# Optimization experiments

Measured on AMD Instinct MI355X. Metric: run time of the kernel, lower is better.

The kernel has to match this reference:

```python
import jax, jax.numpy as jnp
import numpy as np

# ---- dims derived from Decoder(input_size=64, hidden_size=64, output_size=64, n_units=512) ----
B, L, I = 512, 256, 64
N_UNITS, N_MOTOR = 512, 64
N_COMMAND = max(int(0.4 * (N_UNITS - N_MOTOR)), 1)   # 179 (AutoNCP rule)
N_INTER = N_UNITS - N_MOTOR - N_COMMAND              # 269
SENSORY_FANOUT = max(int(N_INTER * 0.5), 1)          # density_level = 0.5
INTER_FANOUT = max(int(N_COMMAND * 0.5), 1)
MOTOR_FANIN = max(int(N_COMMAND * 0.5), 1)


def _make_masks():
    # Binary NCP connectivity (CfCCell uses abs(mask), so polarity is irrelevant).
    rng = np.random.RandomState(22222)
    m0 = np.zeros((I, N_INTER), np.float32)           # sensory -> inter
    for r in range(I):
        m0[r, rng.choice(N_INTER, SENSORY_FANOUT, replace=False)] = 1.0
    m1 = np.zeros((N_INTER, N_COMMAND), np.float32)   # inter -> command
    for r in range(N_INTER):
        m1[r, rng.choice(N_COMMAND, INTER_FANOUT, replace=False)] = 1.0
    m2 = np.zeros((N_COMMAND, N_MOTOR), np.float32)   # command -> motor (fanin per motor)
    for c in range(N_MOTOR):
        m2[rng.choice(N_COMMAND, MOTOR_FANIN, replace=False), c] = 1.0
    # WiredCfCCell: per-layer mask = [input_sparsity ; ones(h,h)]^T -> shape (h, in+h)
    def cellmask(m, h):
        return np.concatenate([m, np.ones((h, h), np.float32)], axis=0).T
    return (jnp.asarray(cellmask(m0, N_INTER)),
            jnp.asarray(cellmask(m1, N_COMMAND)),
            jnp.asarray(cellmask(m2, N_MOTOR)))


def _lin(key, out_f, in_f):
    kw, kb = jax.random.split(key)
    bound = 1.0 / np.sqrt(in_f)
    W = jax.random.uniform(kw, (out_f, in_f), jnp.float32, -bound, bound)
    b = jax.random.uniform(kb, (out_f,), jnp.float32, -bound, bound)
    return W, b


def setup_inputs() -> dict:
    key = jax.random.key(0)
    ks = jax.random.split(key, 8)
    dt = jax.random.uniform(ks[0], (B, L, I), jnp.float32)
    hidden_state = jax.random.normal(ks[1], (B, N_UNITS), jnp.float32) * 0.1
    M0, M1, M2 = _make_masks()
    # Each layer fuses ff1, ff2, time_a, time_b -> one (4h, in+h) weight.
    W0, b0 = _lin(ks[2], 4 * N_INTER, I + N_INTER)
    W1, b1 = _lin(ks[3], 4 * N_COMMAND, N_INTER + N_COMMAND)
    W2, b2 = _lin(ks[4], 4 * N_MOTOR, N_COMMAND + N_MOTOR)
    b0 = b0.reshape(4, N_INTER).reshape(-1)  # no-op, keeps layout explicit
    Wout, bout = _lin(ks[5], N_MOTOR, N_MOTOR)  # nn.Linear(hidden_size=64, output_size=64)
    return {"dt": dt, "hidden_state": hidden_state,
            "W0": W0, "b0": b0, "W1": W1, "b1": b1, "W2": W2, "b2": b2,
            "Wout": Wout, "bout": bout, "M0": M0, "M1": M1, "M2": M2}


def _masked_weight(W, M, h):
    # sparsity mask applies to ff1 and ff2 only; time_a/time_b stay dense
    return jnp.concatenate([W[:h] * M, W[h:2 * h] * M, W[2 * h:]], axis=0)


def _cell(x_in, h, Weff, b):
    # CfC 'default' mode, no backbone, ts = 1.0
    x = jnp.concatenate([x_in, h], axis=-1)
    z = x @ Weff.T + b
    ff1, ff2, ta, tb = jnp.split(z, 4, axis=-1)
    ti = jax.nn.sigmoid(ta * 1.0 + tb)
    return jnp.tanh(ff1) * (1.0 - ti) + ti * jnp.tanh(ff2)


def reference(dt, hidden_state, W0, b0, W1, b1, W2, b2, Wout, bout, M0, M1, M2):
    We0 = _masked_weight(W0, M0, N_INTER)
    We1 = _masked_weight(W1, M1, N_COMMAND)
    We2 = _masked_weight(W2, M2, N_MOTOR)
    h0 = hidden_state[:, :N_INTER]
    h1 = hidden_state[:, N_INTER:N_INTER + N_COMMAND]
    h2 = hidden_state[:, N_INTER + N_COMMAND:]

    def step(carry, x_t):
        a, b_, c = carry
        a = _cell(x_t, a, We0, b0)   # inter layer
        b_ = _cell(a, b_, We1, b1)   # command layer
        c = _cell(b_, c, We2, b2)    # motor layer (CfC output per step)
        return (a, b_, c), c

    _, ys = jax.lax.scan(step, (h0, h1, h2), jnp.swapaxes(dt, 0, 1))
    seq = jnp.swapaxes(ys, 0, 1)          # (B, L, N_MOTOR)
    return seq @ Wout.T + bout            # output_layer
```

## Files before the change

### kernel.cpp

```cpp
#include <hip/hip_runtime.h>
#include <stdint.h>

typedef _Float16 f16x8 __attribute__((ext_vector_type(8)));
typedef unsigned short u16x8 __attribute__((ext_vector_type(8)));
typedef float f32x4 __attribute__((ext_vector_type(4)));
typedef unsigned int u32x4 __attribute__((ext_vector_type(4)));

#define MFMA16(a,b,c) __builtin_amdgcn_mfma_f32_16x16x32_f16((a),(b),(c),0,0,0)

#define LSEQ 256
#define H0N  269
#define H1N  179
#define H0P  272
#define H1P  192
#define K0REAL 333
#define K1REAL 448
#define K2REAL 243
#define KK0  11
#define KK1  15
#define KK2  8
#define XH0S 360
#define XH1S 488
#define XH2S 200
#define MR   32

#define H0_OFF   0
#define H0_SLOT  (MR*H0P*2)
#define H1_OFF   (8*H0_SLOT)
#define H1_SLOT  (MR*H1P*2)
#define C2_OFF   (H1_OFF + 8*H1_SLOT)
#define CNT_OFF  (C2_OFF + 4096)
#define GSTRIDE  262144

#define BIGNEG   (-(1<<28))
#define NQ0 5
#define NQ1 8
#define NQ2 3

__device__ __forceinline__ unsigned short f2h_bits(float v) {
  return __builtin_bit_cast(unsigned short, (_Float16)v);
}
__device__ __forceinline__ float rcpf(float x) { return __builtin_amdgcn_rcpf(x); }
__device__ __forceinline__ float fast_sig(float s) { return rcpf(1.f + __expf(-s)); }
__device__ __forceinline__ float fast_tanh(float x) {
  float e = __expf(2.f * x);
  return 1.f - 2.f * rcpf(e + 1.f);
}

__device__ __forceinline__ u16x8 ldg16s(const unsigned short* p) {
  u16x8 r;
  asm volatile("global_load_dwordx4 %0, %1, off sc0 sc1" : "=v"(r) : "v"(p));
  return r;
}
__device__ __forceinline__ void stg16s(unsigned short* p, u16x8 v) {
  asm volatile("global_store_dwordx4 %0, %1, off sc0 sc1" :: "v"(p), "v"(v) : "memory");
}
__device__ __forceinline__ unsigned ld_flag(const unsigned int* p) {
  unsigned v;
  asm volatile("global_load_dword %0, %1, off sc0 sc1" : "=v"(v) : "v"(p) : "memory");
  return v;
}
__device__ __forceinline__ void st_flag(unsigned int* p, unsigned v) {
  asm volatile("global_store_dword %0, %1, off sc0 sc1" :: "v"(p), "v"(v) : "memory");
}
#define VM_WAIT0 do { asm volatile("s_waitcnt vmcnt(0)" ::: "memory"); __builtin_amdgcn_sched_barrier(0); } while (0)

__device__ __forceinline__ bool chunk_fresh(u16x8 v, unsigned tp) {
  u32x4 d = __builtin_bit_cast(u32x4, v);
  return ((d[0] & 0x00010001u) == tp) & ((d[1] & 0x00010001u) == tp) &
         ((d[2] & 0x00010001u) == tp) & ((d[3] & 0x00010001u) == tp);
}
__device__ __forceinline__ u16x8 tag_chunk(u16x8 v, unsigned tp) {
  u32x4 d = __builtin_bit_cast(u32x4, v);
  d &= 0xFFFEFFFEu;
  d |= tp;
  return __builtin_bit_cast(u16x8, d);
}

__global__ void __launch_bounds__(256) init_state(const float* __restrict__ hs, char* __restrict__ ws) {
  int g = blockIdx.x, tid = threadIdx.x;
  char* gb = ws + (size_t)g * GSTRIDE;
  uint4 z4 = {0,0,0,0};
  int total16 = (CNT_OFF + 512) / 16;
  for (int i = tid; i < total16; i += 256) ((uint4*)gb)[i] = z4;
  __syncthreads();
  int b0 = g * MR;
  unsigned short* H0 = (unsigned short*)(gb + H0_OFF + 7*(size_t)H0_SLOT);
  unsigned short* H1 = (unsigned short*)(gb + H1_OFF + 7*(size_t)H1_SLOT);
  unsigned short* C2 = (unsigned short*)(gb + C2_OFF);
  for (int i = tid; i < MR*H0P; i += 256) { int r = i/H0P, c = i%H0P;
    H0[i] = (c < H0N) ? (unsigned short)(f2h_bits(hs[(size_t)(b0+r)*512 + c]) & 0xFFFEu) : (unsigned short)0; }
  for (int i = tid; i < MR*H1P; i += 256) { int r = i/H1P, c = i%H1P;
    H1[i] = (c < H1N) ? (unsigned short)(f2h_bits(hs[(size_t)(b0+r)*512 + H0N + c]) & 0xFFFEu) : (unsigned short)0; }
  for (int i = tid; i < MR*64;  i += 256) { int r = i>>6,  c = i&63;
    C2[i] = f2h_bits(hs[(size_t)(b0+r)*512 + 448 + c]); }
}

template<int KK, int MODE>
__device__ __forceinline__ void build_frag3(f16x8* wf, const float* __restrict__ W, const float* __restrict__ Msk,
                                            int h, int Kreal, int g4, int tile, int lane) {
  int col = tile * 16 + (lane & 15);
  bool nv = (col < h);
  #pragma unroll
  for (int kk = 0; kk < KK; ++kk) {
    f16x8 s;
    #pragma unroll
    for (int e = 0; e < 8; ++e) {
      int k = kk*32 + ((lane >> 4) << 3) + e;
      int wc;
      if (MODE == 0)      wc = (k < 333) ? k : -1;
      else if (MODE == 1) wc = (k < 269) ? k : ((k >= 272 && k < 451) ? (k - 3) : -1);
      else                wc = (k < 179) ? k : ((k >= 192 && k < 256) ? (k - 13) : -1);
      float val = 0.f;
      if (nv && wc >= 0) {
        if (g4 < 2) val = W[(size_t)(g4 * h + col) * Kreal + wc] * Msk[(size_t)col * Kreal + wc];
        else        val = W[(size_t)(2 * h + col) * Kreal + wc] + W[(size_t)(3 * h + col) * Kreal + wc];
      }
      s[e] = (_Float16)val;
    }
    wf[kk] = s;
  }
}

__device__ __forceinline__ f16x8 lda(const unsigned short* xh, int stride, int mt, int kk, int lane) {
  const unsigned short* p = xh + (size_t)(mt*16 + (lane & 15)) * stride + kk*32 + ((lane >> 4) << 3);
  return __builtin_bit_cast(f16x8, *(const u16x8*)p);
}

__global__ void __launch_bounds__(256, 1) rnn_persist(
    const float* __restrict__ dt,
    const float* __restrict__ W0, const float* __restrict__ b0v,
    const float* __restrict__ W1, const float* __restrict__ b1v,
    const float* __restrict__ W2, const float* __restrict__ b2v,
    const float* __restrict__ Wout, const float* __restrict__ boutg,
    const float* __restrict__ M0, const float* __restrict__ M1, const float* __restrict__ M2,
    float* __restrict__ out, char* __restrict__ ws)
{
  __shared__ __attribute__((aligned(16))) unsigned short xhS[MR * XH1S];
  __shared__ __attribute__((aligned(16))) unsigned short hbuf[4][32][16];

  int tid = threadIdx.x;
  int lane = tid & 63, wave = tid >> 6;
  int bid = blockIdx.x;
  int j = bid >> 4;
  int g = bid & 15;
  int b0 = g * MR;

  char* gb = ws + (size_t)g * GSTRIDE;
  unsigned short* H0r = (unsigned short*)(gb + H0_OFF);
  unsigned short* H1r = (unsigned short*)(gb + H1_OFF);
  unsigned int*   cnt = (unsigned int*)(gb + CNT_OFF);
  u16x8 zz = {0,0,0,0,0,0,0,0};

  if (j < 5) {
    int tile = j*4 + wave;
    bool act = (tile < 17);
    int ncol = tile*16 + (lane & 15);
    bool cok = act && (ncol < H0N);
    f16x8 wf[3][KK0];
    if (act) {
      #pragma unroll
      for (int g4 = 0; g4 < 3; ++g4) build_frag3<KK0,0>(wf[g4], W0, M0, H0N, K0REAL, g4, tile, lane);
    }
    float bb[3] = {0.f,0.f,0.f};
    if (cok) {
      bb[0] = b0v[ncol]; bb[1] = b0v[H0N + ncol];
      bb[2] = b0v[2*H0N + ncol] + b0v[3*H0N + ncol];
    }
    if (tid < 64) {
      int r = tid >> 1, c8 = 336 + (tid & 1)*8;
      *(u16x8*)(xhS + (size_t)r*XH0S + c8) = zz;
    }
    int aoff[NQ0], adst[NQ0]; bool aval[NQ0];
    #pragma unroll
    for (int q = 0; q < NQ0; ++q) {
      int idx = tid + q*256;
      aval[q] = (idx < MR*34);
      int r = idx / 34, cc = (idx % 34) * 8;
      aoff[q] = r*H0P + cc;
      adst[q] = r*XH0S + 64 + cc;
    }
    int xrow = tid >> 3, xc = (tid & 7) * 8;
    const float* dtb = dt + ((size_t)(b0 + xrow) * LSEQ) * 64 + xc;
    float4 xA = *(const float4*)(dtb);
    float4 xB = *(const float4*)(dtb + 4);
    int goff = (lane < 5) ? -6 : (lane < 8) ? -7 : BIGNEG;
    for (int t = 0; t < LSEQ; ++t) {
      unsigned tpm1 = (((unsigned)(t + 7) >> 3) & 1) * 0x00010001u;
      unsigned tpt  = (((unsigned)(t + 8) >> 3) & 1) * 0x00010001u;
      {
        unsigned short* d = xhS + (size_t)xrow*XH0S + xc;
        d[0]=f2h_bits(xA.x); d[1]=f2h_bits(xA.y); d[2]=f2h_bits(xA.z); d[3]=f2h_bits(xA.w);
        d[4]=f2h_bits(xB.x); d[5]=f2h_bits(xB.y); d[6]=f2h_bits(xB.z); d[7]=f2h_bits(xB.w);
      }
      const unsigned short* H0s = H0r + (size_t)((t + 7) & 7) * (MR*H0P);
      u16x8 tA[NQ0];
      for (int it = 0; it < (1 << 17); ++it) {
        unsigned gv = 0;
        if (lane < 8) gv = ld_flag(cnt + lane);
        #pragma unroll
        for (int q = 0; q < NQ0; ++q) if (aval[q]) tA[q] = ldg16s(H0s + aoff[q]);
        VM_WAIT0;
        bool ok = ((int)gv >= t + goff);
        #pragma unroll
        for (int q = 0; q < NQ0; ++q) if (aval[q]) ok &= chunk_fresh(tA[q], tpm1);
        if (__all(ok)) break;
        __builtin_amdgcn_s_sleep(1);
      }
      #pragma unroll
      for (int q = 0; q < NQ0; ++q) if (aval[q]) *(u16x8*)(xhS + adst[q]) = tA[q];
      __syncthreads();
      if (tid == 0) st_flag(&cnt[j], t + 1);
      { int tn = (t + 1 < LSEQ) ? t + 1 : t;
        xA = *(const float4*)(dtb + (size_t)tn*64);
        xB = *(const float4*)(dtb + (size_t)tn*64 + 4); }
      f32x4 ac[3][2];
      if (act) {
        #pragma unroll
        for (int g4 = 0; g4 < 3; ++g4) { ac[g4][0] = (f32x4){0,0,0,0}; ac[g4][1] = (f32x4){0,0,0,0}; }
        #pragma unroll
        for (int kk = 0; kk < KK0; ++kk) {
          f16x8 a0 = lda(xhS, XH0S, 0, kk, lane);
          f16x8 a1 = lda(xhS, XH0S, 1, kk, lane);
          #pragma unroll
          for (int g4 = 0; g4 < 3; ++g4) {
            ac[g4][0] = MFMA16(a0, wf[g4][kk], ac[g4][0]);
            ac[g4][1] = MFMA16(a1, wf[g4][kk], ac[g4][1]);
          }
        }
      }
      __syncthreads();
      if (act) {
        #pragma unroll
        for (int m = 0; m < 2; ++m) {
          #pragma unroll
          for (int r = 0; r < 4; ++r) {
            float ti = fast_sig(ac[2][m][r] + bb[2]);
            float hv = cok ? (fast_tanh(ac[0][m][r] + bb[0])*(1.f - ti) + ti*fast_tanh(ac[1][m][r] + bb[1])) : 0.f;
            hbuf[wave][m*16 + (lane>>4)*4 + r][lane & 15] = f2h_bits(hv);
          }
        }
        int row = lane >> 1, c8v = (lane & 1) * 8;
        u16x8 hv8 = tag_chunk(*(const u16x8*)&hbuf[wave][row][c8v], tpt);
        unsigned short* Hn = H0r + (size_t)(t & 7) * (MR*H0P);
        stg16s(Hn + (size_t)row*H0P + tile*16 + c8v, hv8);
      }
    }
  } else if (j < 8) {
    int tile = (j - 5)*4 + wave;
    int ncol = tile*16 + (lane & 15);
    bool cok = (ncol < H1N);
    f16x8 wf[3][KK1];
    #pragma unroll
    for (int g4 = 0; g4 < 3; ++g4) build_frag3<KK1,1>(wf[g4], W1, M1, H1N, K1REAL, g4, tile, lane);
    float bb[3] = {0.f,0.f,0.f};
    if (cok) {
      bb[0] = b1v[ncol]; bb[1] = b1v[H1N + ncol];
      bb[2] = b1v[2*H1N + ncol] + b1v[3*H1N + ncol];
    }
    if (tid < 64) {
      int r = tid >> 1, c8 = 464 + (tid & 1)*8;
      *(u16x8*)(xhS + (size_t)r*XH1S + c8) = zz;
    }
    int soff[NQ1], sdst[NQ1]; bool sval[NQ1], sisB[NQ1];
    #pragma unroll
    for (int q = 0; q < NQ1; ++q) {
      int idx = tid + q*256;
      if (idx < 1088) {
        sval[q] = true; sisB[q] = false;
        int r = idx / 34, cc = (idx % 34) * 8;
        soff[q] = r*H0P + cc; sdst[q] = r*XH1S + cc;
      } else {
        int i2 = idx - 1088;
        sval[q] = (i2 < 768); sisB[q] = true;
        int r = i2 / 24, cc = (i2 % 24) * 8;
        soff[q] = r*H1P + cc; sdst[q] = r*XH1S + 272 + cc;
      }
    }
    int goff = (lane >= 5 && lane < 8) ? -6 : (lane == 8) ? -7 : BIGNEG;
    for (int t = 0; t < LSEQ; ++t) {
      unsigned tpm1 = (((unsigned)(t + 7) >> 3) & 1) * 0x00010001u;
      unsigned tpt  = (((unsigned)(t + 8) >> 3) & 1) * 0x00010001u;
      const unsigned short* As = H0r + (size_t)(t & 7) * (MR*H0P);
      const unsigned short* Bs = H1r + (size_t)((t + 7) & 7) * (MR*H1P);
      u16x8 tS[NQ1];
      for (int it = 0; it < (1 << 17); ++it) {
        unsigned gv = 0;
        if (lane >= 5 && lane < 9) gv = ld_flag(cnt + lane);
        #pragma unroll
        for (int q = 0; q < NQ1; ++q) if (sval[q]) tS[q] = ldg16s((sisB[q] ? Bs : As) + soff[q]);
        VM_WAIT0;
        bool ok = ((int)gv >= t + goff);
        #pragma unroll
        for (int q = 0; q < NQ1; ++q) if (sval[q]) ok &= chunk_fresh(tS[q], sisB[q] ? tpm1 : tpt);
        if (__all(ok)) break;
        __builtin_amdgcn_s_sleep(1);
      }
      #pragma unroll
      for (int q = 0; q < NQ1; ++q) if (sval[q]) *(u16x8*)(xhS + sdst[q]) = tS[q];
      __syncthreads();
      if (tid == 0) st_flag(&cnt[j], t + 1);
      f32x4 ac[3][2];
      #pragma unroll
      for (int g4 = 0; g4 < 3; ++g4) { ac[g4][0] = (f32x4){0,0,0,0}; ac[g4][1] = (f32x4){0,0,0,0}; }
      #pragma unroll
      for (int kk = 0; kk < KK1; ++kk) {
        f16x8 a0 = lda(xhS, XH1S, 0, kk, lane);
        f16x8 a1 = lda(xhS, XH1S, 1, kk, lane);
        #pragma unroll
        for (int g4 = 0; g4 < 3; ++g4) {
          ac[g4][0] = MFMA16(a0, wf[g4][kk], ac[g4][0]);
          ac[g4][1] = MFMA16(a1, wf[g4][kk], ac[g4][1]);
        }
      }
      __syncthreads();
      {
        #pragma unroll
        for (int m = 0; m < 2; ++m) {
          #pragma unroll
          for (int r = 0; r < 4; ++r) {
            float ti = fast_sig(ac[2][m][r] + bb[2]);
            float hv = cok ? (fast_tanh(ac[0][m][r] + bb[0])*(1.f - ti) + ti*fast_tanh(ac[1][m][r] + bb[1])) : 0.f;
            hbuf[wave][m*16 + (lane>>4)*4 + r][lane & 15] = f2h_bits(hv);
          }
        }
        int row = lane >> 1, c8v = (lane & 1) * 8;
        u16x8 hv8 = tag_chunk(*(const u16x8*)&hbuf[wave][row][c8v], tpt);
        unsigned short* Hn = H1r + (size_t)(t & 7) * (MR*H1P);
        stg16s(Hn + (size_t)row*H1P + tile*16 + c8v, hv8);
      }
    }
  } else {
    int tile = wave;
    int ncol = tile*16 + (lane & 15);
    f16x8 wf[3][KK2], woutf[2];
    #pragma unroll
    for (int g4 = 0; g4 < 3; ++g4) build_frag3<KK2,2>(wf[g4], W2, M2, 64, K2REAL, g4, tile, lane);
    {
      #pragma unroll
      for (int kk = 0; kk < 2; ++kk) {
        f16x8 s;
        #pragma unroll
        for (int e = 0; e < 8; ++e) {
          int k = kk*32 + ((lane >> 4) << 3) + e;
          s[e] = (_Float16)Wout[(size_t)ncol*64 + k];
        }
        woutf[kk] = s;
      }
    }
    float bov = boutg[ncol];
    float bb[3];
    bb[0] = b2v[ncol]; bb[1] = b2v[64 + ncol];
    bb[2] = b2v[2*64 + ncol] + b2v[3*64 + ncol];
    {
      const unsigned short* C2i = (const unsigned short*)(gb + C2_OFF);
      int r = tid >> 3, c8 = (tid & 7) * 8;
      u16x8 cv = ldg16s(C2i + r*64 + c8);
      VM_WAIT0;
      *(u16x8*)&hbuf[c8 >> 4][r][c8 & 15] = cv;
    }
    int soff[NQ2], sdst[NQ2];
    #pragma unroll
    for (int q = 0; q < NQ2; ++q) {
      int idx = tid + q*256;
      int r = idx / 24, cc = (idx % 24) * 8;
      soff[q] = r*H1P + cc; sdst[q] = r*XH2S + cc;
    }
    for (int t = 0; t < LSEQ; ++t) {
      unsigned tpt = (((unsigned)(t + 8) >> 3) & 1) * 0x00010001u;
      const unsigned short* Bs = H1r + (size_t)(t & 7) * (MR*H1P);
      u16x8 tS[NQ2];
      for (int it = 0; it < (1 << 17); ++it) {
        #pragma unroll
        for (int q = 0; q < NQ2; ++q) tS[q] = ldg16s(Bs + soff[q]);
        VM_WAIT0;
        bool ok = true;
        #pragma unroll
        for (int q = 0; q < NQ2; ++q) ok &= chunk_fresh(tS[q], tpt);
        if (__all(ok)) break;
        __builtin_amdgcn_s_sleep(1);
      }
      #pragma unroll
      for (int q = 0; q < NQ2; ++q) *(u16x8*)(xhS + sdst[q]) = tS[q];
      __syncthreads();
      if (tid == 0) st_flag(&cnt[8], t + 1);
      f32x4 ac[3][2];
      #pragma unroll
      for (int g4 = 0; g4 < 3; ++g4) { ac[g4][0] = (f32x4){0,0,0,0}; ac[g4][1] = (f32x4){0,0,0,0}; }
      #pragma unroll
      for (int kk = 0; kk < KK2; ++kk) {
        f16x8 a0, a1;
        if (kk < 6) {
          a0 = lda(xhS, XH2S, 0, kk, lane);
          a1 = lda(xhS, XH2S, 1, kk, lane);
        } else {
          int k0 = kk*32 + ((lane >> 4) << 3) - 192;
          a0 = __builtin_bit_cast(f16x8, *(const u16x8*)&hbuf[k0 >> 4][(lane & 15)][k0 & 15]);
          a1 = __builtin_bit_cast(f16x8, *(const u16x8*)&hbuf[k0 >> 4][16 + (lane & 15)][k0 & 15]);
        }
        #pragma unroll
        for (int g4 = 0; g4 < 3; ++g4) {
          ac[g4][0] = MFMA16(a0, wf[g4][kk], ac[g4][0]);
          ac[g4][1] = MFMA16(a1, wf[g4][kk], ac[g4][1]);
        }
      }
      __syncthreads();
      {
        #pragma unroll
        for (int m = 0; m < 2; ++m) {
          #pragma unroll
          for (int r = 0; r < 4; ++r) {
            float ti = fast_sig(ac[2][m][r] + bb[2]);
            float hv = fast_tanh(ac[0][m][r] + bb[0])*(1.f - ti) + ti*fast_tanh(ac[1][m][r] + bb[1]);
            hbuf[wave][m*16 + (lane>>4)*4 + r][lane & 15] = f2h_bits(hv);
          }
        }
      }
      __syncthreads();
      {
        #pragma unroll
        for (int m = 0; m < 2; ++m) {
          f32x4 acc = {0.f,0.f,0.f,0.f};
          #pragma unroll
          for (int kk = 0; kk < 2; ++kk) {
            int k0 = kk*32 + ((lane >> 4) << 3);
            f16x8 a = __builtin_bit_cast(f16x8, *(const u16x8*)&hbuf[k0 >> 4][m*16 + (lane & 15)][k0 & 15]);
            acc = MFMA16(a, woutf[kk], acc);
          }
          int cc = lane & 15, rb = (lane >> 4) * 4;
          #pragma unroll
          for (int r = 0; r < 4; ++r) {
            int row = m*16 + rb + r;
            out[((size_t)(b0 + row) * LSEQ + t) * 64 + tile*16 + cc] = acc[r] + bov;
          }
        }
      }
    }
  }
}

extern "C" void kernel_launch(void* const* d_in, const int* in_sizes, int n_in,
                              void* d_out, int out_size, void* d_ws, size_t ws_size,
                              hipStream_t stream) {
  const float* dt   = (const float*)d_in[0];
  const float* hs   = (const float*)d_in[1];
  const float* W0   = (const float*)d_in[2];
  const float* b0v  = (const float*)d_in[3];
  const float* W1   = (const float*)d_in[4];
  const float* b1v  = (const float*)d_in[5];
  const float* W2   = (const float*)d_in[6];
  const float* b2v  = (const float*)d_in[7];
  const float* Wo   = (const float*)d_in[8];
  const float* bo   = (const float*)d_in[9];
  const float* M0   = (const float*)d_in[10];
  const float* M1   = (const float*)d_in[11];
  const float* M2   = (const float*)d_in[12];
  (void)in_sizes; (void)n_in; (void)out_size; (void)ws_size;
  init_state<<<16, 256, 0, stream>>>(hs, (char*)d_ws);
  rnn_persist<<<144, 256, 0, stream>>>(dt, W0, b0v, W1, b1v, W2, b2v, Wo, bo, M0, M1, M2,
                                       (float*)d_out, (char*)d_ws);
}
```

Before: 1.064 ms.

## Load MFMA A-fragments directly from global and sync per wave

In the inter and command layers, each wave now loads its MFMA A-operand fragments straight from the global hidden-state ring into registers. It no longer stages them through shared memory, which removes the block-wide __syncthreads barriers. Progress flags are published per wave tile instead of per block, and consumers poll the individual tile counters. This shortens the serial per-step critical path, at the cost of redundant global loads across waves and more polling lanes.

```diff
diff --git a/kernel.cpp b/kernel.cpp
--- a/kernel.cpp
+++ b/kernel.cpp
@@ -7,6 +7,7 @@
 typedef unsigned int u32x4 __attribute__((ext_vector_type(4)));
 
 #define MFMA16(a,b,c) __builtin_amdgcn_mfma_f32_16x16x32_f16((a),(b),(c),0,0,0)
+#define F16(v) __builtin_bit_cast(f16x8, (v))
 
 #define LSEQ 256
 #define H0N  269
@@ -19,8 +20,6 @@
 #define KK0  11
 #define KK1  15
 #define KK2  8
-#define XH0S 360
-#define XH1S 488
 #define XH2S 200
 #define MR   32
 
@@ -33,8 +32,6 @@
 #define GSTRIDE  262144
 
 #define BIGNEG   (-(1<<28))
-#define NQ0 5
-#define NQ1 8
 #define NQ2 3
 
 __device__ __forceinline__ unsigned short f2h_bits(float v) {
@@ -75,6 +72,12 @@
   d &= 0xFFFEFFFEu;
   d |= tp;
   return __builtin_bit_cast(u16x8, d);
+}
+__device__ __forceinline__ f16x8 cvt8(float4 a, float4 b) {
+  f16x8 s;
+  s[0]=(_Float16)a.x; s[1]=(_Float16)a.y; s[2]=(_Float16)a.z; s[3]=(_Float16)a.w;
+  s[4]=(_Float16)b.x; s[5]=(_Float16)b.y; s[6]=(_Float16)b.z; s[7]=(_Float16)b.w;
+  return s;
 }
 
 __global__ void __launch_bounds__(256) init_state(const float* __restrict__ hs, char* __restrict__ ws) {
@@ -136,7 +139,7 @@
     const float* __restrict__ M0, const float* __restrict__ M1, const float* __restrict__ M2,
     float* __restrict__ out, char* __restrict__ ws)
 {
-  __shared__ __attribute__((aligned(16))) unsigned short xhS[MR * XH1S];
+  __shared__ __attribute__((aligned(16))) unsigned short xhS[MR * XH2S];
   __shared__ __attribute__((aligned(16))) unsigned short hbuf[4][32][16];
 
   int tid = threadIdx.x;
@@ -150,105 +153,108 @@
   unsigned short* H0r = (unsigned short*)(gb + H0_OFF);
   unsigned short* H1r = (unsigned short*)(gb + H1_OFF);
   unsigned int*   cnt = (unsigned int*)(gb + CNT_OFF);
+  int r0 = lane & 15, ks = (lane >> 4) * 8;
   u16x8 zz = {0,0,0,0,0,0,0,0};
 
   if (j < 5) {
     int tile = j*4 + wave;
-    bool act = (tile < 17);
-    int ncol = tile*16 + (lane & 15);
-    bool cok = act && (ncol < H0N);
+    if (tile >= 17) return;
+    int ncol = tile*16 + r0;
+    bool cok = (ncol < H0N);
     f16x8 wf[3][KK0];
-    if (act) {
-      #pragma unroll
-      for (int g4 = 0; g4 < 3; ++g4) build_frag3<KK0,0>(wf[g4], W0, M0, H0N, K0REAL, g4, tile, lane);
-    }
+    #pragma unroll
+    for (int g4 = 0; g4 < 3; ++g4) build_frag3<KK0,0>(wf[g4], W0, M0, H0N, K0REAL, g4, tile, lane);
     float bb[3] = {0.f,0.f,0.f};
     if (cok) {
       bb[0] = b0v[ncol]; bb[1] = b0v[H0N + ncol];
       bb[2] = b0v[2*H0N + ncol] + b0v[3*H0N + ncol];
     }
-    if (tid < 64) {
-      int r = tid >> 1, c8 = 336 + (tid & 1)*8;
-      *(u16x8*)(xhS + (size_t)r*XH0S + c8) = zz;
-    }
-    int aoff[NQ0], adst[NQ0]; bool aval[NQ0];
-    #pragma unroll
-    for (int q = 0; q < NQ0; ++q) {
-      int idx = tid + q*256;
-      aval[q] = (idx < MR*34);
-      int r = idx / 34, cc = (idx % 34) * 8;
-      aoff[q] = r*H0P + cc;
-      adst[q] = r*XH0S + 64 + cc;
-    }
-    int xrow = tid >> 3, xc = (tid & 7) * 8;
-    const float* dtb = dt + ((size_t)(b0 + xrow) * LSEQ) * 64 + xc;
-    float4 xA = *(const float4*)(dtb);
-    float4 xB = *(const float4*)(dtb + 4);
-    int goff = (lane < 5) ? -6 : (lane < 8) ? -7 : BIGNEG;
+    u16x8 tA[2][9];
+    bool hval[9];
+    #pragma unroll
+    for (int q = 0; q < 9; ++q) {
+      hval[q] = ((q + 2)*32 + ks - 64) < 272;
+      tA[0][q] = zz; tA[1][q] = zz;
+    }
+    const float* xp0 = dt + (size_t)(b0 + r0) * (LSEQ*64);
+    const float* xp1 = dt + (size_t)(b0 + r0 + 16) * (LSEQ*64);
+    float4 xs[8];
+    #pragma unroll
+    for (int c = 0; c < 2; ++c) {
+      xs[c*2]   = *(const float4*)(xp0 + c*32 + ks);
+      xs[c*2+1] = *(const float4*)(xp0 + c*32 + ks + 4);
+      xs[4+c*2]   = *(const float4*)(xp1 + c*32 + ks);
+      xs[4+c*2+1] = *(const float4*)(xp1 + c*32 + ks + 4);
+    }
+    int gt_base = (lane < 17) ? -6 : (lane >= 20 && lane < 32) ? -7 : BIGNEG;
     for (int t = 0; t < LSEQ; ++t) {
       unsigned tpm1 = (((unsigned)(t + 7) >> 3) & 1) * 0x00010001u;
       unsigned tpt  = (((unsigned)(t + 8) >> 3) & 1) * 0x00010001u;
-      {
-        unsigned short* d = xhS + (size_t)xrow*XH0S + xc;
-        d[0]=f2h_bits(xA.x); d[1]=f2h_bits(xA.y); d[2]=f2h_bits(xA.z); d[3]=f2h_bits(xA.w);
-        d[4]=f2h_bits(xB.x); d[5]=f2h_bits(xB.y); d[6]=f2h_bits(xB.z); d[7]=f2h_bits(xB.w);
-      }
       const unsigned short* H0s = H0r + (size_t)((t + 7) & 7) * (MR*H0P);
-      u16x8 tA[NQ0];
+      const unsigned short* row0 = H0s + (size_t)r0 * H0P;
+      const unsigned short* row1 = H0s + (size_t)(r0 + 16) * H0P;
+      int gt = t + gt_base;
       for (int it = 0; it < (1 << 17); ++it) {
         unsigned gv = 0;
-        if (lane < 8) gv = ld_flag(cnt + lane);
-        #pragma unroll
-        for (int q = 0; q < NQ0; ++q) if (aval[q]) tA[q] = ldg16s(H0s + aoff[q]);
+        if (gt_base != BIGNEG) gv = ld_flag(cnt + lane);
+        #pragma unroll
+        for (int q = 0; q < 9; ++q) {
+          if (hval[q]) {
+            tA[0][q] = ldg16s(row0 + (q + 2)*32 + ks - 64);
+            tA[1][q] = ldg16s(row1 + (q + 2)*32 + ks - 64);
+          }
+        }
         VM_WAIT0;
-        bool ok = ((int)gv >= t + goff);
-        #pragma unroll
-        for (int q = 0; q < NQ0; ++q) if (aval[q]) ok &= chunk_fresh(tA[q], tpm1);
+        bool ok = ((int)gv >= gt);
+        #pragma unroll
+        for (int q = 0; q < 9; ++q) if (hval[q]) ok &= chunk_fresh(tA[0][q], tpm1) & chunk_fresh(tA[1][q], tpm1);
         if (__all(ok)) break;
         __builtin_amdgcn_s_sleep(1);
       }
-      #pragma unroll
-      for (int q = 0; q < NQ0; ++q) if (aval[q]) *(u16x8*)(xhS + adst[q]) = tA[q];
-      __syncthreads();
-      if (tid == 0) st_flag(&cnt[j], t + 1);
-      { int tn = (t + 1 < LSEQ) ? t + 1 : t;
-        xA = *(const float4*)(dtb + (size_t)tn*64);
-        xB = *(const float4*)(dtb + (size_t)tn*64 + 4); }
+      if (lane == 0) st_flag(&cnt[tile], t + 1);
+      f16x8 xf[2][2];
+      xf[0][0] = cvt8(xs[0], xs[1]); xf[1][0] = cvt8(xs[2], xs[3]);
+      xf[0][1] = cvt8(xs[4], xs[5]); xf[1][1] = cvt8(xs[6], xs[7]);
+      {
+        int tn = (t + 1 < LSEQ) ? t + 1 : t;
+        #pragma unroll
+        for (int c = 0; c < 2; ++c) {
+          xs[c*2]   = *(const float4*)(xp0 + (size_t)tn*64 + c*32 + ks);
+          xs[c*2+1] = *(const float4*)(xp0 + (size_t)tn*64 + c*32 + ks + 4);
+          xs[4+c*2]   = *(const float4*)(xp1 + (size_t)tn*64 + c*32 + ks);
+          xs[4+c*2+1] = *(const float4*)(xp1 + (size_t)tn*64 + c*32 + ks + 4);
+        }
+      }
       f32x4 ac[3][2];
-      if (act) {
-        #pragma unroll
-        for (int g4 = 0; g4 < 3; ++g4) { ac[g4][0] = (f32x4){0,0,0,0}; ac[g4][1] = (f32x4){0,0,0,0}; }
-        #pragma unroll
-        for (int kk = 0; kk < KK0; ++kk) {
-          f16x8 a0 = lda(xhS, XH0S, 0, kk, lane);
-          f16x8 a1 = lda(xhS, XH0S, 1, kk, lane);
-          #pragma unroll
-          for (int g4 = 0; g4 < 3; ++g4) {
-            ac[g4][0] = MFMA16(a0, wf[g4][kk], ac[g4][0]);
-            ac[g4][1] = MFMA16(a1, wf[g4][kk], ac[g4][1]);
-          }
-        }
-      }
-      __syncthreads();
-      if (act) {
-        #pragma unroll
-        for (int m = 0; m < 2; ++m) {
-          #pragma unroll
-          for (int r = 0; r < 4; ++r) {
-            float ti = fast_sig(ac[2][m][r] + bb[2]);
-            float hv = cok ? (fast_tanh(ac[0][m][r] + bb[0])*(1.f - ti) + ti*fast_tanh(ac[1][m][r] + bb[1])) : 0.f;
-            hbuf[wave][m*16 + (lane>>4)*4 + r][lane & 15] = f2h_bits(hv);
-          }
-        }
-        int row = lane >> 1, c8v = (lane & 1) * 8;
-        u16x8 hv8 = tag_chunk(*(const u16x8*)&hbuf[wave][row][c8v], tpt);
-        unsigned short* Hn = H0r + (size_t)(t & 7) * (MR*H0P);
-        stg16s(Hn + (size_t)row*H0P + tile*16 + c8v, hv8);
-      }
+      #pragma unroll
+      for (int g4 = 0; g4 < 3; ++g4) { ac[g4][0] = (f32x4){0,0,0,0}; ac[g4][1] = (f32x4){0,0,0,0}; }
+      #pragma unroll
+      for (int kk = 0; kk < KK0; ++kk) {
+        f16x8 a0 = (kk < 2) ? xf[kk][0] : F16(tA[0][kk-2]);
+        f16x8 a1 = (kk < 2) ? xf[kk][1] : F16(tA[1][kk-2]);
+        #pragma unroll
+        for (int g4 = 0; g4 < 3; ++g4) {
+          ac[g4][0] = MFMA16(a0, wf[g4][kk], ac[g4][0]);
+          ac[g4][1] = MFMA16(a1, wf[g4][kk], ac[g4][1]);
+        }
+      }
+      #pragma unroll
+      for (int m = 0; m < 2; ++m) {
+        #pragma unroll
+        for (int r = 0; r < 4; ++r) {
+          float ti = fast_sig(ac[2][m][r] + bb[2]);
+          float hv = cok ? (fast_tanh(ac[0][m][r] + bb[0])*(1.f - ti) + ti*fast_tanh(ac[1][m][r] + bb[1])) : 0.f;
+          hbuf[wave][m*16 + (lane>>4)*4 + r][r0] = f2h_bits(hv);
+        }
+      }
+      int srow = lane >> 1, c8v = (lane & 1) * 8;
+      u16x8 hv8 = tag_chunk(*(const u16x8*)&hbuf[wave][srow][c8v], tpt);
+      unsigned short* Hn = H0r + (size_t)(t & 7) * (MR*H0P);
+      stg16s(Hn + (size_t)srow*H0P + tile*16 + c8v, hv8);
     }
   } else if (j < 8) {
     int tile = (j - 5)*4 + wave;
-    int ncol = tile*16 + (lane & 15);
+    int ncol = tile*16 + r0;
     bool cok = (ncol < H1N);
     f16x8 wf[3][KK1];
     #pragma unroll
@@ -258,81 +264,81 @@
       bb[0] = b1v[ncol]; bb[1] = b1v[H1N + ncol];
       bb[2] = b1v[2*H1N + ncol] + b1v[3*H1N + ncol];
     }
-    if (tid < 64) {
-      int r = tid >> 1, c8 = 464 + (tid & 1)*8;
-      *(u16x8*)(xhS + (size_t)r*XH1S + c8) = zz;
-    }
-    int soff[NQ1], sdst[NQ1]; bool sval[NQ1], sisB[NQ1];
-    #pragma unroll
-    for (int q = 0; q < NQ1; ++q) {
-      int idx = tid + q*256;
-      if (idx < 1088) {
-        sval[q] = true; sisB[q] = false;
-        int r = idx / 34, cc = (idx % 34) * 8;
-        soff[q] = r*H0P + cc; sdst[q] = r*XH1S + cc;
-      } else {
-        int i2 = idx - 1088;
-        sval[q] = (i2 < 768); sisB[q] = true;
-        int r = i2 / 24, cc = (i2 % 24) * 8;
-        soff[q] = r*H1P + cc; sdst[q] = r*XH1S + 272 + cc;
-      }
-    }
-    int goff = (lane >= 5 && lane < 8) ? -6 : (lane == 8) ? -7 : BIGNEG;
+    u16x8 tS[2][KK1];
+    bool isa[KK1], val[KK1];
+    int coff[KK1];
+    #pragma unroll
+    for (int kk = 0; kk < KK1; ++kk) {
+      int k = kk*32 + ks;
+      isa[kk] = (k < 272);
+      val[kk] = (k < 464);
+      coff[kk] = isa[kk] ? k : (k - 272);
+      tS[0][kk] = zz; tS[1][kk] = zz;
+    }
+    int gt_base = (lane >= 20 && lane < 32) ? -6 : (lane == 32) ? -7 : BIGNEG;
     for (int t = 0; t < LSEQ; ++t) {
       unsigned tpm1 = (((unsigned)(t + 7) >> 3) & 1) * 0x00010001u;
       unsigned tpt  = (((unsigned)(t + 8) >> 3) & 1) * 0x00010001u;
       const unsigned short* As = H0r + (size_t)(t & 7) * (MR*H0P);
       const unsigned short* Bs = H1r + (size_t)((t + 7) & 7) * (MR*H1P);
-      u16x8 tS[NQ1];
+      const unsigned short* ar0 = As + (size_t)r0 * H0P;
+      const unsigned short* ar1 = As + (size_t)(r0 + 16) * H0P;
+      const unsigned short* br0 = Bs + (size_t)r0 * H1P;
+      const unsigned short* br1 = Bs + (size_t)(r0 + 16) * H1P;
+      int gt = t + gt_base;
       for (int it = 0; it < (1 << 17); ++it) {
         unsigned gv = 0;
-        if (lane >= 5 && lane < 9) gv = ld_flag(cnt + lane);
-        #pragma unroll
-        for (int q = 0; q < NQ1; ++q) if (sval[q]) tS[q] = ldg16s((sisB[q] ? Bs : As) + soff[q]);
+        if (gt_base != BIGNEG) gv = ld_flag(cnt + lane);
+        #pragma unroll
+        for (int kk = 0; kk < KK1; ++kk) {
+          if (val[kk]) {
+            tS[0][kk] = ldg16s((isa[kk] ? ar0 : br0) + coff[kk]);
+            tS[1][kk] = ldg16s((isa[kk] ? ar1 : br1) + coff[kk]);
+          }
+        }
         VM_WAIT0;
-        bool ok = ((int)gv >= t + goff);
-        #pragma unroll
-        for (int q = 0; q < NQ1; ++q) if (sval[q]) ok &= chunk_fresh(tS[q], sisB[q] ? tpm1 : tpt);
+        bool ok = ((int)gv >= gt);
+        #pragma unroll
+        for (int kk = 0; kk < KK1; ++kk) {
+          if (val[kk]) {
+            unsigned tp = isa[kk] ? tpt : tpm1;
+            ok &= chunk_fresh(tS[0][kk], tp) & chunk_fresh(tS[1][kk], tp);
+          }
+        }
         if (__all(ok)) break;
         __builtin_amdgcn_s_sleep(1);
       }
-      #pragma unroll
-      for (int q = 0; q < NQ1; ++q) if (sval[q]) *(u16x8*)(xhS + sdst[q]) = tS[q];
-      __syncthreads();
-      if (tid == 0) st_flag(&cnt[j], t + 1);
+      if (lane == 0) st_flag(&cnt[20 + tile], t + 1);
       f32x4 ac[3][2];
       #pragma unroll
       for (int g4 = 0; g4 < 3; ++g4) { ac[g4][0] = (f32x4){0,0,0,0}; ac[g4][1] = (f32x4){0,0,0,0}; }
       #pragma unroll
       for (int kk = 0; kk < KK1; ++kk) {
-        f16x8 a0 = lda(xhS, XH1S, 0, kk, lane);
-        f16x8 a1 = lda(xhS, XH1S, 1, kk, lane);
+        f16x8 a0 = F16(tS[0][kk]);
+        f16x8 a1 = F16(tS[1][kk]);
         #pragma unroll
         for (int g4 = 0; g4 < 3; ++g4) {
           ac[g4][0] = MFMA16(a0, wf[g4][kk], ac[g4][0]);
           ac[g4][1] = MFMA16(a1, wf[g4][kk], ac[g4][1]);
         }
       }
-      __syncthreads();
-      {
-        #pragma unroll
-        for (int m = 0; m < 2; ++m) {
-          #pragma unroll
-          for (int r = 0; r < 4; ++r) {
-            float ti = fast_sig(ac[2][m][r] + bb[2]);
-            float hv = cok ? (fast_tanh(ac[0][m][r] + bb[0])*(1.f - ti) + ti*fast_tanh(ac[1][m][r] + bb[1])) : 0.f;
-            hbuf[wave][m*16 + (lane>>4)*4 + r][lane & 15] = f2h_bits(hv);
-          }
-        }
-        int row = lane >> 1, c8v = (lane & 1) * 8;
-        u16x8 hv8 = tag_chunk(*(const u16x8*)&hbuf[wave][row][c8v], tpt);
-        unsigned short* Hn = H1r + (size_t)(t & 7) * (MR*H1P);
-        stg16s(Hn + (size_t)row*H1P + tile*16 + c8v, hv8);
-      }
+      #pragma unroll
+      for (int m = 0; m < 2; ++m) {
+        #pragma unroll
+        for (int r = 0; r < 4; ++r) {
+          float ti = fast_sig(ac[2][m][r] + bb[2]);
+          float hv = cok ? (fast_tanh(ac[0][m][r] + bb[0])*(1.f - ti) + ti*fast_tanh(ac[1][m][r] + bb[1])) : 0.f;
+          hbuf[wave][m*16 + (lane>>4)*4 + r][r0] = f2h_bits(hv);
+        }
+      }
+      int srow = lane >> 1, c8v = (lane & 1) * 8;
+      u16x8 hv8 = tag_chunk(*(const u16x8*)&hbuf[wave][srow][c8v], tpt);
+      unsigned short* Hn = H1r + (size_t)(t & 7) * (MR*H1P);
+      stg16s(Hn + (size_t)srow*H1P + tile*16 + c8v, hv8);
     }
   } else {
     int tile = wave;
-    int ncol = tile*16 + (lane & 15);
+    int ncol = tile*16 + r0;
     f16x8 wf[3][KK2], woutf[2];
     #pragma unroll
     for (int g4 = 0; g4 < 3; ++g4) build_frag3<KK2,2>(wf[g4], W2, M2, 64, K2REAL, g4, tile, lane);
@@ -342,7 +348,7 @@
         f16x8 s;
         #pragma unroll
         for (int e = 0; e < 8; ++e) {
-          int k = kk*32 + ((lane >> 4) << 3) + e;
+          int k = kk*32 + ks + e;
           s[e] = (_Float16)Wout[(size_t)ncol*64 + k];
         }
         woutf[kk] = s;
@@ -383,7 +389,7 @@
       #pragma unroll
       for (int q = 0; q < NQ2; ++q) *(u16x8*)(xhS + sdst[q]) = tS[q];
       __syncthreads();
-      if (tid == 0) st_flag(&cnt[8], t + 1);
+      if (tid == 0) st_flag(&cnt[32], t + 1);
       f32x4 ac[3][2];
       #pragma unroll
       for (int g4 = 0; g4 < 3; ++g4) { ac[g4][0] = (f32x4){0,0,0,0}; ac[g4][1] = (f32x4){0,0,0,0}; }
@@ -394,9 +400,9 @@
           a0 = lda(xhS, XH2S, 0, kk, lane);
           a1 = lda(xhS, XH2S, 1, kk, lane);
         } else {
-          int k0 = kk*32 + ((lane >> 4) << 3) - 192;
-          a0 = __builtin_bit_cast(f16x8, *(const u16x8*)&hbuf[k0 >> 4][(lane & 15)][k0 & 15]);
-          a1 = __builtin_bit_cast(f16x8, *(const u16x8*)&hbuf[k0 >> 4][16 + (lane & 15)][k0 & 15]);
+          int k0 = kk*32 + ks - 192;
+          a0 = __builtin_bit_cast(f16x8, *(const u16x8*)&hbuf[k0 >> 4][r0][k0 & 15]);
+          a1 = __builtin_bit_cast(f16x8, *(const u16x8*)&hbuf[k0 >> 4][16 + r0][k0 & 15]);
         }
         #pragma unroll
         for (int g4 = 0; g4 < 3; ++g4) {
@@ -412,7 +418,7 @@
           for (int r = 0; r < 4; ++r) {
             float ti = fast_sig(ac[2][m][r] + bb[2]);
             float hv = fast_tanh(ac[0][m][r] + bb[0])*(1.f - ti) + ti*fast_tanh(ac[1][m][r] + bb[1]);
-            hbuf[wave][m*16 + (lane>>4)*4 + r][lane & 15] = f2h_bits(hv);
+            hbuf[wave][m*16 + (lane>>4)*4 + r][r0] = f2h_bits(hv);
           }
         }
       }
@@ -423,15 +429,15 @@
           f32x4 acc = {0.f,0.f,0.f,0.f};
           #pragma unroll
           for (int kk = 0; kk < 2; ++kk) {
-            int k0 = kk*32 + ((lane >> 4) << 3);
-            f16x8 a = __builtin_bit_cast(f16x8, *(const u16x8*)&hbuf[k0 >> 4][m*16 + (lane & 15)][k0 & 15]);
+            int k0 = kk*32 + ks;
+            f16x8 a = __builtin_bit_cast(f16x8, *(const u16x8*)&hbuf[k0 >> 4][m*16 + r0][k0 & 15]);
             acc = MFMA16(a, woutf[kk], acc);
           }
-          int cc = lane & 15, rb = (lane >> 4) * 4;
+          int rb = (lane >> 4) * 4;
           #pragma unroll
           for (int r = 0; r < 4; ++r) {
             int row = m*16 + rb + r;
-            out[((size_t)(b0 + row) * LSEQ + t) * 64 + tile*16 + cc] = acc[r] + bov;
+            out[((size_t)(b0 + row) * LSEQ + t) * 64 + tile*16 + r0] = acc[r] + bov;
           }
         }
       }
```

Result: slower. 2.536 ms (+138.3%).

## Double rows per block group to 64, halving batch groups and blocks

Applied to the files above, without the earlier changes.

Raises the batch rows each block group handles from 32 to 64, so there are 8 groups and 72 persistent blocks instead of 16 and 144. Each wave now runs four M-tiles of MFMA per step, reusing the register-resident weight fragments over twice as many rows. The change reduces the number of blocks spinning on global flags and the cross-block synchronisation traffic per row. In exchange, per-step latency grows, because each block does twice the MFMA and elementwise work on the serial recurrence critical path. It also uses fewer CUs, so less of the GPU is busy.

```diff
diff --git a/kernel.cpp b/kernel.cpp
--- a/kernel.cpp
+++ b/kernel.cpp
@@ -7,6 +7,7 @@
 typedef unsigned int u32x4 __attribute__((ext_vector_type(4)));
 
 #define MFMA16(a,b,c) __builtin_amdgcn_mfma_f32_16x16x32_f16((a),(b),(c),0,0,0)
+#define F16(v) __builtin_bit_cast(f16x8, (v))
 
 #define LSEQ 256
 #define H0N  269
@@ -22,20 +23,20 @@
 #define XH0S 360
 #define XH1S 488
 #define XH2S 200
-#define MR   32
+#define MR   64
 
 #define H0_OFF   0
 #define H0_SLOT  (MR*H0P*2)
 #define H1_OFF   (8*H0_SLOT)
 #define H1_SLOT  (MR*H1P*2)
 #define C2_OFF   (H1_OFF + 8*H1_SLOT)
-#define CNT_OFF  (C2_OFF + 4096)
-#define GSTRIDE  262144
+#define CNT_OFF  (C2_OFF + MR*64*2)
+#define GSTRIDE  524288
 
 #define BIGNEG   (-(1<<28))
-#define NQ0 5
-#define NQ1 8
-#define NQ2 3
+#define NQ0 9
+#define NQ1 15
+#define NQ2 6
 
 __device__ __forceinline__ unsigned short f2h_bits(float v) {
   return __builtin_bit_cast(unsigned short, (_Float16)v);
@@ -137,25 +138,26 @@
     float* __restrict__ out, char* __restrict__ ws)
 {
   __shared__ __attribute__((aligned(16))) unsigned short xhS[MR * XH1S];
-  __shared__ __attribute__((aligned(16))) unsigned short hbuf[4][32][16];
+  __shared__ __attribute__((aligned(16))) unsigned short hbuf[4][MR][16];
 
   int tid = threadIdx.x;
   int lane = tid & 63, wave = tid >> 6;
   int bid = blockIdx.x;
-  int j = bid >> 4;
-  int g = bid & 15;
+  int j = bid >> 3;
+  int g = bid & 7;
   int b0 = g * MR;
 
   char* gb = ws + (size_t)g * GSTRIDE;
   unsigned short* H0r = (unsigned short*)(gb + H0_OFF);
   unsigned short* H1r = (unsigned short*)(gb + H1_OFF);
   unsigned int*   cnt = (unsigned int*)(gb + CNT_OFF);
+  int r0 = lane & 15;
   u16x8 zz = {0,0,0,0,0,0,0,0};
 
   if (j < 5) {
     int tile = j*4 + wave;
     bool act = (tile < 17);
-    int ncol = tile*16 + (lane & 15);
+    int ncol = tile*16 + r0;
     bool cok = act && (ncol < H0N);
     f16x8 wf[3][KK0];
     if (act) {
@@ -167,7 +169,7 @@
       bb[0] = b0v[ncol]; bb[1] = b0v[H0N + ncol];
       bb[2] = b0v[2*H0N + ncol] + b0v[3*H0N + ncol];
     }
-    if (tid < 64) {
+    if (tid < 128) {
       int r = tid >> 1, c8 = 336 + (tid & 1)*8;
       *(u16x8*)(xhS + (size_t)r*XH0S + c8) = zz;
     }
@@ -181,17 +183,21 @@
       adst[q] = r*XH0S + 64 + cc;
     }
     int xrow = tid >> 3, xc = (tid & 7) * 8;
-    const float* dtb = dt + ((size_t)(b0 + xrow) * LSEQ) * 64 + xc;
-    float4 xA = *(const float4*)(dtb);
-    float4 xB = *(const float4*)(dtb + 4);
+    const float* dtb0 = dt + ((size_t)(b0 + xrow) * LSEQ) * 64 + xc;
+    const float* dtb1 = dtb0 + (size_t)32 * LSEQ * 64;
+    float4 xA0 = *(const float4*)(dtb0), xB0 = *(const float4*)(dtb0 + 4);
+    float4 xA1 = *(const float4*)(dtb1), xB1 = *(const float4*)(dtb1 + 4);
     int goff = (lane < 5) ? -6 : (lane < 8) ? -7 : BIGNEG;
     for (int t = 0; t < LSEQ; ++t) {
       unsigned tpm1 = (((unsigned)(t + 7) >> 3) & 1) * 0x00010001u;
       unsigned tpt  = (((unsigned)(t + 8) >> 3) & 1) * 0x00010001u;
       {
-        unsigned short* d = xhS + (size_t)xrow*XH0S + xc;
-        d[0]=f2h_bits(xA.x); d[1]=f2h_bits(xA.y); d[2]=f2h_bits(xA.z); d[3]=f2h_bits(xA.w);
-        d[4]=f2h_bits(xB.x); d[5]=f2h_bits(xB.y); d[6]=f2h_bits(xB.z); d[7]=f2h_bits(xB.w);
+        unsigned short* d0 = xhS + (size_t)xrow*XH0S + xc;
+        unsigned short* d1 = xhS + (size_t)(xrow + 32)*XH0S + xc;
+        d0[0]=f2h_bits(xA0.x); d0[1]=f2h_bits(xA0.y); d0[2]=f2h_bits(xA0.z); d0[3]=f2h_bits(xA0.w);
+        d0[4]=f2h_bits(xB0.x); d0[5]=f2h_bits(xB0.y); d0[6]=f2h_bits(xB0.z); d0[7]=f2h_bits(xB0.w);
+        d1[0]=f2h_bits(xA1.x); d1[1]=f2h_bits(xA1.y); d1[2]=f2h_bits(xA1.z); d1[3]=f2h_bits(xA1.w);
+        d1[4]=f2h_bits(xB1.x); d1[5]=f2h_bits(xB1.y); d1[6]=f2h_bits(xB1.z); d1[7]=f2h_bits(xB1.w);
       }
       const unsigned short* H0s = H0r + (size_t)((t + 7) & 7) * (MR*H0P);
       u16x8 tA[NQ0];
@@ -212,43 +218,51 @@
       __syncthreads();
       if (tid == 0) st_flag(&cnt[j], t + 1);
       { int tn = (t + 1 < LSEQ) ? t + 1 : t;
-        xA = *(const float4*)(dtb + (size_t)tn*64);
-        xB = *(const float4*)(dtb + (size_t)tn*64 + 4); }
-      f32x4 ac[3][2];
+        xA0 = *(const float4*)(dtb0 + (size_t)tn*64);
+        xB0 = *(const float4*)(dtb0 + (size_t)tn*64 + 4);
+        xA1 = *(const float4*)(dtb1 + (size_t)tn*64);
+        xB1 = *(const float4*)(dtb1 + (size_t)tn*64 + 4); }
+      f32x4 ac[3][4];
       if (act) {
         #pragma unroll
-        for (int g4 = 0; g4 < 3; ++g4) { ac[g4][0] = (f32x4){0,0,0,0}; ac[g4][1] = (f32x4){0,0,0,0}; }
+        for (int g4 = 0; g4 < 3; ++g4) {
+          #pragma unroll
+          for (int m = 0; m < 4; ++m) ac[g4][m] = (f32x4){0,0,0,0};
+        }
         #pragma unroll
         for (int kk = 0; kk < KK0; ++kk) {
-          f16x8 a0 = lda(xhS, XH0S, 0, kk, lane);
-          f16x8 a1 = lda(xhS, XH0S, 1, kk, lane);
-          #pragma unroll
-          for (int g4 = 0; g4 < 3; ++g4) {
-            ac[g4][0] = MFMA16(a0, wf[g4][kk], ac[g4][0]);
-            ac[g4][1] = MFMA16(a1, wf[g4][kk], ac[g4][1]);
+          #pragma unroll
+          for (int m = 0; m < 4; ++m) {
+            f16x8 a = lda(xhS, XH0S, m, kk, lane);
+            #pragma unroll
+            for (int g4 = 0; g4 < 3; ++g4) ac[g4][m] = MFMA16(a, wf[g4][kk], ac[g4][m]);
           }
         }
       }
       __syncthreads();
       if (act) {
         #pragma unroll
-        for (int m = 0; m < 2; ++m) {
+        for (int m = 0; m < 4; ++m) {
           #pragma unroll
           for (int r = 0; r < 4; ++r) {
             float ti = fast_sig(ac[2][m][r] + bb[2]);
             float hv = cok ? (fast_tanh(ac[0][m][r] + bb[0])*(1.f - ti) + ti*fast_tanh(ac[1][m][r] + bb[1])) : 0.f;
-            hbuf[wave][m*16 + (lane>>4)*4 + r][lane & 15] = f2h_bits(hv);
-          }
-        }
-        int row = lane >> 1, c8v = (lane & 1) * 8;
-        u16x8 hv8 = tag_chunk(*(const u16x8*)&hbuf[wave][row][c8v], tpt);
+            hbuf[wave][m*16 + (lane>>4)*4 + r][r0] = f2h_bits(hv);
+          }
+        }
         unsigned short* Hn = H0r + (size_t)(t & 7) * (MR*H0P);
-        stg16s(Hn + (size_t)row*H0P + tile*16 + c8v, hv8);
+        int c8v = (lane & 1) * 8;
+        #pragma unroll
+        for (int s = 0; s < 2; ++s) {
+          int srow = s*32 + (lane >> 1);
+          u16x8 hv8 = tag_chunk(*(const u16x8*)&hbuf[wave][srow][c8v], tpt);
+          stg16s(Hn + (size_t)srow*H0P + tile*16 + c8v, hv8);
+        }
       }
     }
   } else if (j < 8) {
     int tile = (j - 5)*4 + wave;
-    int ncol = tile*16 + (lane & 15);
+    int ncol = tile*16 + r0;
     bool cok = (ncol < H1N);
     f16x8 wf[3][KK1];
     #pragma unroll
@@ -258,7 +272,7 @@
       bb[0] = b1v[ncol]; bb[1] = b1v[H1N + ncol];
       bb[2] = b1v[2*H1N + ncol] + b1v[3*H1N + ncol];
     }
-    if (tid < 64) {
+    if (tid < 128) {
       int r = tid >> 1, c8 = 464 + (tid & 1)*8;
       *(u16x8*)(xhS + (size_t)r*XH1S + c8) = zz;
     }
@@ -266,13 +280,13 @@
     #pragma unroll
     for (int q = 0; q < NQ1; ++q) {
       int idx = tid + q*256;
-      if (idx < 1088) {
+      if (idx < MR*34) {
         sval[q] = true; sisB[q] = false;
         int r = idx / 34, cc = (idx % 34) * 8;
         soff[q] = r*H0P + cc; sdst[q] = r*XH1S + cc;
       } else {
-        int i2 = idx - 1088;
-        sval[q] = (i2 < 768); sisB[q] = true;
+        int i2 = idx - MR*34;
+        sval[q] = (i2 < MR*24); sisB[q] = true;
         int r = i2 / 24, cc = (i2 % 24) * 8;
         soff[q] = r*H1P + cc; sdst[q] = r*XH1S + 272 + cc;
       }
@@ -292,7 +306,9 @@
         VM_WAIT0;
         bool ok = ((int)gv >= t + goff);
         #pragma unroll
-        for (int q = 0; q < NQ1; ++q) if (sval[q]) ok &= chunk_fresh(tS[q], sisB[q] ? tpm1 : tpt);
+        for (int q = 0; q < NQ1; ++q) {
+          if (sval[q]) ok &= chunk_fresh(tS[q], sisB[q] ? tpm1 : tpt);
+        }
         if (__all(ok)) break;
         __builtin_amdgcn_s_sleep(1);
       }
@@ -300,39 +316,46 @@
       for (int q = 0; q < NQ1; ++q) if (sval[q]) *(u16x8*)(xhS + sdst[q]) = tS[q];
       __syncthreads();
       if (tid == 0) st_flag(&cnt[j], t + 1);
-      f32x4 ac[3][2];
-      #pragma unroll
-      for (int g4 = 0; g4 < 3; ++g4) { ac[g4][0] = (f32x4){0,0,0,0}; ac[g4][1] = (f32x4){0,0,0,0}; }
+      f32x4 ac[3][4];
+      #pragma unroll
+      for (int g4 = 0; g4 < 3; ++g4) {
+        #pragma unroll
+        for (int m = 0; m < 4; ++m) ac[g4][m] = (f32x4){0,0,0,0};
+      }
       #pragma unroll
       for (int kk = 0; kk < KK1; ++kk) {
-        f16x8 a0 = lda(xhS, XH1S, 0, kk, lane);
-        f16x8 a1 = lda(xhS, XH1S, 1, kk, lane);
-        #pragma unroll
-        for (int g4 = 0; g4 < 3; ++g4) {
-          ac[g4][0] = MFMA16(a0, wf[g4][kk], ac[g4][0]);
-          ac[g4][1] = MFMA16(a1, wf[g4][kk], ac[g4][1]);
+        #pragma unroll
+        for (int m = 0; m < 4; ++m) {
+          f16x8 a = lda(xhS, XH1S, m, kk, lane);
+          #pragma unroll
+          for (int g4 = 0; g4 < 3; ++g4) ac[g4][m] = MFMA16(a, wf[g4][kk], ac[g4][m]);
         }
       }
       __syncthreads();
       {
         #pragma unroll
-        for (int m = 0; m < 2; ++m) {
+        for (int m = 0; m < 4; ++m) {
           #pragma unroll
           for (int r = 0; r < 4; ++r) {
             float ti = fast_sig(ac[2][m][r] + bb[2]);
             float hv = cok ? (fast_tanh(ac[0][m][r] + bb[0])*(1.f - ti) + ti*fast_tanh(ac[1][m][r] + bb[1])) : 0.f;
-            hbuf[wave][m*16 + (lane>>4)*4 + r][lane & 15] = f2h_bits(hv);
-          }
-        }
-        int row = lane >> 1, c8v = (lane & 1) * 8;
-        u16x8 hv8 = tag_chunk(*(const u16x8*)&hbuf[wave][row][c8v], tpt);
+            hbuf[wave][m*16 + (lane>>4)*4 + r][r0] = f2h_bits(hv);
+          }
+        }
         unsigned short* Hn = H1r + (size_t)(t & 7) * (MR*H1P);
-        stg16s(Hn + (size_t)row*H1P + tile*16 + c8v, hv8);
+        int c8v = (lane & 1) * 8;
+        #pragma unroll
+        for (int s = 0; s < 2; ++s) {
+          int srow = s*32 + (lane >> 1);
+          u16x8 hv8 = tag_chunk(*(const u16x8*)&hbuf[wave][srow][c8v], tpt);
+          stg16s(Hn + (size_t)srow*H1P + tile*16 + c8v, hv8);
+        }
       }
     }
   } else {
     int tile = wave;
-    int ncol = tile*16 + (lane & 15);
+    int ncol = tile*16 + r0;
+    int ks = (lane >> 4) * 8;
     f16x8 wf[3][KK2], woutf[2];
     #pragma unroll
     for (int g4 = 0; g4 < 3; ++g4) build_frag3<KK2,2>(wf[g4], W2, M2, 64, K2REAL, g4, tile, lane);
@@ -342,7 +365,7 @@
         f16x8 s;
         #pragma unroll
         for (int e = 0; e < 8; ++e) {
-          int k = kk*32 + ((lane >> 4) << 3) + e;
+          int k = kk*32 + ks + e;
           s[e] = (_Float16)Wout[(size_t)ncol*64 + k];
         }
         woutf[kk] = s;
@@ -354,10 +377,14 @@
     bb[2] = b2v[2*64 + ncol] + b2v[3*64 + ncol];
     {
       const unsigned short* C2i = (const unsigned short*)(gb + C2_OFF);
-      int r = tid >> 3, c8 = (tid & 7) * 8;
-      u16x8 cv = ldg16s(C2i + r*64 + c8);
-      VM_WAIT0;
-      *(u16x8*)&hbuf[c8 >> 4][r][c8 & 15] = cv;
+      #pragma unroll
+      for (int q = 0; q < 2; ++q) {
+        int idx = tid + q*256;
+        int r = idx >> 3, c8 = (idx & 7) * 8;
+        u16x8 cv = ldg16s(C2i + r*64 + c8);
+        VM_WAIT0;
+        *(u16x8*)&hbuf[c8 >> 4][r][c8 & 15] = cv;
+      }
     }
     int soff[NQ2], sdst[NQ2];
     #pragma unroll
@@ -384,54 +411,55 @@
       for (int q = 0; q < NQ2; ++q) *(u16x8*)(xhS + sdst[q]) = tS[q];
       __syncthreads();
       if (tid == 0) st_flag(&cnt[8], t + 1);
-      f32x4 ac[3][2];
-      #pragma unroll
-      for (int g4 = 0; g4 < 3; ++g4) { ac[g4][0] = (f32x4){0,0,0,0}; ac[g4][1] = (f32x4){0,0,0,0}; }
+      f32x4 ac[3][4];
+      #pragma unroll
+      for (int g4 = 0; g4 < 3; ++g4) {
+        #pragma unroll
+        for (int m = 0; m < 4; ++m) ac[g4][m] = (f32x4){0,0,0,0};
+      }
       #pragma unroll
       for (int kk = 0; kk < KK2; ++kk) {
-        f16x8 a0, a1;
-        if (kk < 6) {
-          a0 = lda(xhS, XH2S, 0, kk, lane);
-          a1 = lda(xhS, XH2S, 1, kk, lane);
-        } else {
-          int k0 = kk*32 + ((lane >> 4) << 3) - 192;
-          a0 = __builtin_bit_cast(f16x8, *(const u16x8*)&hbuf[k0 >> 4][(lane & 15)][k0 & 15]);
-          a1 = __builtin_bit_cast(f16x8, *(const u16x8*)&hbuf[k0 >> 4][16 + (lane & 15)][k0 & 15]);
-        }
-        #pragma unroll
-        for (int g4 = 0; g4 < 3; ++g4) {
-          ac[g4][0] = MFMA16(a0, wf[g4][kk], ac[g4][0]);
-          ac[g4][1] = MFMA16(a1, wf[g4][kk], ac[g4][1]);
+        #pragma unroll
+        for (int m = 0; m < 4; ++m) {
+          f16x8 a;
+          if (kk < 6) {
+            a = lda(xhS, XH2S, m, kk, lane);
+          } else {
+            int k0 = kk*32 + ks - 192;
+            a = __builtin_bit_cast(f16x8, *(const u16x8*)&hbuf[k0 >> 4][m*16 + r0][k0 & 15]);
+          }
+          #pragma unroll
+          for (int g4 = 0; g4 < 3; ++g4) ac[g4][m] = MFMA16(a, wf[g4][kk], ac[g4][m]);
         }
       }
       __syncthreads();
       {
         #pragma unroll
-        for (int m = 0; m < 2; ++m) {
+        for (int m = 0; m < 4; ++m) {
           #pragma unroll
           for (int r = 0; r < 4; ++r) {
             float ti = fast_sig(ac[2][m][r] + bb[2]);
             float hv = fast_tanh(ac[0][m][r] + bb[0])*(1.f - ti) + ti*fast_tanh(ac[1][m][r] + bb[1]);
-            hbuf[wave][m*16 + (lane>>4)*4 + r][lane & 15] = f2h_bits(hv);
+            hbuf[wave][m*16 + (lane>>4)*4 + r][r0] = f2h_bits(hv);
           }
         }
       }
       __syncthreads();
       {
         #pragma unroll
-        for (int m = 0; m < 2; ++m) {
+        for (int m = 0; m < 4; ++m) {
           f32x4 acc = {0.f,0.f,0.f,0.f};
           #pragma unroll
           for (int kk = 0; kk < 2; ++kk) {
-            int k0 = kk*32 + ((lane >> 4) << 3);
-            f16x8 a = __builtin_bit_cast(f16x8, *(const u16x8*)&hbuf[k0 >> 4][m*16 + (lane & 15)][k0 & 15]);
+            int k0 = kk*32 + ks;
+            f16x8 a = __builtin_bit_cast(f16x8, *(const u16x8*)&hbuf[k0 >> 4][m*16 + r0][k0 & 15]);
             acc = MFMA16(a, woutf[kk], acc);
           }
-          int cc = lane & 15, rb = (lane >> 4) * 4;
+          int rb = (lane >> 4) * 4;
           #pragma unroll
           for (int r = 0; r < 4; ++r) {
             int row = m*16 + rb + r;
-            out[((size_t)(b0 + row) * LSEQ + t) * 64 + tile*16 + cc] = acc[r] + bov;
+            out[((size_t)(b0 + row) * LSEQ + t) * 64 + tile*16 + r0] = acc[r] + bov;
           }
         }
       }
@@ -456,7 +484,7 @@
   const float* M1   = (const float*)d_in[11];
   const float* M2   = (const float*)d_in[12];
   (void)in_sizes; (void)n_in; (void)out_size; (void)ws_size;
-  init_state<<<16, 256, 0, stream>>>(hs, (char*)d_ws);
-  rnn_persist<<<144, 256, 0, stream>>>(dt, W0, b0v, W1, b1v, W2, b2v, Wo, bo, M0, M1, M2,
-                                       (float*)d_out, (char*)d_ws);
-}
+  init_state<<<8, 256, 0, stream>>>(hs, (char*)d_ws);
+  rnn_persist<<<72, 256, 0, stream>>>(dt, W0, b0v, W1, b1v, W2, b2v, Wo, bo, M0, M1, M2,
+                                      (float*)d_out, (char*)d_ws);
+}
```

Measured after the change: 1.922 ms. 80.6% more time.
